# Performance work log

Hardware: AMD Instinct MI355X
Metric: run time of the kernel (lower is better)

Reference implementation:

```python
import jax, jax.numpy as jnp
import numpy as np
from jax import lax

B = 4096
IM = 64
HID = 256          # LSTM hidden
OBS_D = 400        # obs embedding dim
SAMP_D = 16        # sample embedding dim
ADDR_D = 16        # address embedding dim
IN_D = OBS_D + SAMP_D + ADDR_D  # 432 LSTM input dim


def setup_inputs() -> dict:
    key = jax.random.key(0)
    ks = jax.random.split(key, 32)
    n = jax.random.normal
    s = 0.05
    return {
        "obs": n(ks[0], (B, IM, IM), jnp.float32),
        "program_id": jax.random.randint(ks[1], (B,), 0, 3),
        "shape_id": jax.random.randint(ks[2], (B,), 0, 2),
        "shape_id_0": jax.random.randint(ks[3], (B,), 0, 2),
        "shape_id_1": jax.random.randint(ks[4], (B,), 0, 2),
        "eps_rp": n(ks[5], (B, 2), jnp.float32),
        "eps_rp0": n(ks[6], (B, 2), jnp.float32),
        "eps_rp1": n(ks[7], (B, 2), jnp.float32),
        # CNN obs embedder (stand-in for util.init_cnn(output_dim=16), flattening to 400)
        "conv1_w": n(ks[8], (32, 1, 3, 3)) * s,
        "conv1_b": n(ks[9], (32,)) * s,
        "conv2_w": n(ks[10], (16, 32, 3, 3)) * s,
        "conv2_b": n(ks[11], (16,)) * s,
        # raw_position_embedder: MLP 2 -> 100 -> 100 -> 16
        "mlp_w1": n(ks[12], (100, 2)) * s,
        "mlp_b1": n(ks[13], (100,)) * s,
        "mlp_w2": n(ks[14], (100, 100)) * s,
        "mlp_b2": n(ks[15], (100,)) * s,
        "mlp_w3": n(ks[16], (SAMP_D, 100)) * s,
        "mlp_b3": n(ks[17], (SAMP_D,)) * s,
        # LSTMCell params (PyTorch layout: [4H, in], gate order i,f,g,o)
        "W_ih": n(ks[18], (4 * HID, IN_D)) * s,
        "b_ih": n(ks[19], (4 * HID,)) * s,
        "W_hh": n(ks[20], (4 * HID, HID)) * s,
        "b_hh": n(ks[21], (4 * HID,)) * s,
        "addr_emb": n(ks[22], (7, ADDR_D)),
        "pid_emb": n(ks[23], (3, SAMP_D)),
        "sid_emb": n(ks[24], (2, SAMP_D)),
        "pid_ext_w": n(ks[25], (3, HID)) * s,
        "pid_ext_b": n(ks[26], (3,)) * s,
        "sid_ext_w": n(ks[27], (2, HID)) * s,
        "sid_ext_b": n(ks[28], (2,)) * s,
        "rp_ext_w": n(ks[29], (4, HID)) * s,
        "rp_ext_b": n(ks[30], (4,)) * s,
    }


def reference(obs, program_id, shape_id, shape_id_0, shape_id_1, eps_rp, eps_rp0, eps_rp1,
              conv1_w, conv1_b, conv2_w, conv2_b,
              mlp_w1, mlp_b1, mlp_w2, mlp_b2, mlp_w3, mlp_b3,
              W_ih, b_ih, W_hh, b_hh,
              addr_emb, pid_emb, sid_emb,
              pid_ext_w, pid_ext_b, sid_ext_w, sid_ext_b, rp_ext_w, rp_ext_b):
    b = obs.shape[0]
    # obs embedder: [B,1,64,64] -> conv s2 -> conv s2 -> avgpool 3x3 -> [B,16,5,5] -> [B,400]
    x = obs[:, None]
    x = jax.nn.relu(lax.conv_general_dilated(x, conv1_w, (2, 2), ((1, 1), (1, 1))) + conv1_b[None, :, None, None])
    x = jax.nn.relu(lax.conv_general_dilated(x, conv2_w, (2, 2), ((1, 1), (1, 1))) + conv2_b[None, :, None, None])
    x = lax.reduce_window(x, 0.0, lax.add, (1, 1, 3, 3), (1, 1, 3, 3), 'VALID') / 9.0
    obs_emb = x.reshape(b, OBS_D)

    def step(samp, aid, h, c):
        a = jnp.broadcast_to(addr_emb[aid], (b, ADDR_D))
        xin = jnp.concatenate([obs_emb, samp, a], axis=-1)
        g = xin @ W_ih.T + b_ih + h @ W_hh.T + b_hh
        i, f, gg, o = jnp.split(g, 4, axis=-1)
        c2 = jax.nn.sigmoid(f) * c + jax.nn.sigmoid(i) * jnp.tanh(gg)
        return jax.nn.sigmoid(o) * jnp.tanh(c2), c2

    zs = jnp.zeros((b, SAMP_D), obs.dtype)
    zh = jnp.zeros((b, HID), obs.dtype)
    h0, c0 = step(zs, 0, zh, zh)
    pid_logits = h0 @ pid_ext_w.T + pid_ext_b
    prev_pid = pid_emb[program_id]

    # branch 0 (program_id == 0): shape_id then raw_position
    h1, c1 = step(prev_pid, 1, h0, c0)
    sid_logits = h1 @ sid_ext_w.T + sid_ext_b
    h2, _ = step(sid_emb[shape_id], 4, h1, c1)
    rp = h2 @ rp_ext_w.T + rp_ext_b
    rp_b0 = rp[:, :2] + jnp.exp(rp[:, 2:]) * eps_rp

    # branch 1 (program_id != 0): shape_id_0, shape_id_1, raw_position_0, raw_position_1
    h1b, c1b = step(prev_pid, 2, h0, c0)
    sid0_logits = h1b @ sid_ext_w.T + sid_ext_b
    h2b, c2b = step(sid_emb[shape_id_0], 3, h1b, c1b)
    sid1_logits = h2b @ sid_ext_w.T + sid_ext_b
    h3b, c3b = step(sid_emb[shape_id_1], 5, h2b, c2b)
    rp0p = h3b @ rp_ext_w.T + rp_ext_b
    rp0 = rp0p[:, :2] + jnp.exp(rp0p[:, 2:]) * eps_rp0
    z = jnp.tanh(rp0 @ mlp_w1.T + mlp_b1)
    z = jnp.tanh(z @ mlp_w2.T + mlp_b2)
    rp0_emb = z @ mlp_w3.T + mlp_b3
    h4b, _ = step(rp0_emb, 6, h3b, c3b)
    rp1p = h4b @ rp_ext_w.T + rp_ext_b
    rp1 = rp1p[:, :2] + jnp.exp(rp1p[:, 2:]) * eps_rp1

    # [B, 3+2+2+2+2+2+2] = [B, 15]
    return jnp.concatenate([pid_logits, sid_logits, rp_b0, sid0_logits, sid1_logits, rp0, rp1], axis=-1)
```

## Files before the change

kernel.cpp:

```cpp
#include <hip/hip_runtime.h>
#include <hip/hip_bf16.h>
#include <math.h>

#define BATCH 4096
#define HID 256
#define OUT_W 15
#define AK 448

typedef unsigned short ushort_t;
typedef unsigned int uint_t;

using bf16x8 = __attribute__((ext_vector_type(8))) short;
using f32x4v = __attribute__((ext_vector_type(4))) float;
using f32x2 = __attribute__((ext_vector_type(2))) float;

__device__ __forceinline__ float sigf(float x) { return 1.0f / (1.0f + __expf(-x)); }
__device__ __forceinline__ float tanh_fast(float x) { return 1.0f - 2.0f / (__expf(2.0f * x) + 1.0f); }
__device__ __forceinline__ float bf2f(ushort_t u) { return __uint_as_float(((uint_t)u) << 16); }
__device__ __forceinline__ ushort_t f2bf(float x) {
    uint_t b = __float_as_uint(x);
    return (ushort_t)((b + 0x7fffu + ((b >> 16) & 1u)) >> 16);
}

__global__ __launch_bounds__(256) void prep_kernel(
// ... 108 lines not shown
    __shared__ __align__(16) float w1s[320];
    const int b = blockIdx.x, t = threadIdx.x;
    const float* og = obs + (size_t)b * 4096;

    const int w = t >> 6, L = t & 63, q = L >> 4, ln = L & 15;

    {
        uint_t* zE = (uint_t*)cE;
        uint_t* zO = (uint_t*)cO;
        for (int i = t; i < CE_RS / 2; i += 512) zE[i] = 0;
        for (int i = t; i < CO_RS / 2; i += 512) zO[i] = 0;
        if (t < 320) {
            int row = (t / 20) + 1, d = t % 20;
            zO[row * (CO_RS / 2) + d] = 0;
        }
    }
    if (t < 80) ((float4*)w1s)[t] = ((const float4*)w1pp)[t];
    if (t < 33) {
        int sw = (t >> 1) & 1;
        sm2[t * SM2S + sw * 4 + 3] = 0.f;
    }

    auto stage_obs = [&](int ph) {
        for (int i = t; i < 33 * 16; i += 512) {
            int row = i >> 4, c4 = i & 15;
            int sw = (row >> 1) & 1;
            int orow = 32 * ph - 1 + row;
            float4 v = float4{0.f, 0.f, 0.f, 0.f};
            if (orow >= 0) v = ((const float4*)(og + (size_t)orow * 64))[c4];
            *(float4*)&sm2[row * SM2S + ((1 + c4) ^ sw) * 4] = v;
        }
    };

    auto conv1_phase = [&](int ph) {
        const int r = t >> 5, g = (t >> 2) & 7, icq = t & 3;
        const int brow = ph ? r : (r + 1);
        float Pt[3][12];
        #pragma unroll
        for (int d = 0; d < 3; d++) {
            int row = 2 * r + d;
            int sw = (row >> 1) & 1;
            const float* base = &sm2[row * SM2S];
            #pragma unroll
            for (int j4 = 0; j4 < 3; j4++) {
                float4 v = *(const float4*)(base + ((2 * g + j4) ^ sw) * 4);
                Pt[d][j4 * 4 + 0] = v.x; Pt[d][j4 * 4 + 1] = v.y;
                Pt[d][j4 * 4 + 2] = v.z; Pt[d][j4 * 4 + 3] = v.w;
            }
        }
        const float* wpbase = &w1s[icq * 80];
        #pragma unroll
        for (int p = 0; p < 4; p++) {
            f32x2 pbc[9];
            #pragma unroll
            for (int d = 0; d < 3; d++)
                #pragma unroll
                for (int dx = 0; dx < 3; dx++) {
                    float v = Pt[d][2 * p + 3 + dx];
                    pbc[d * 3 + dx] = f32x2{v, v};
                }
            f32x2 sall[4];
            #pragma unroll
            for (int i = 0; i < 4; i++) {
                const float* wp = wpbase + i * 20;
                float4 wv0 = *(const float4*)(wp);
                float4 wv1 = *(const float4*)(wp + 4);
                float4 wv2 = *(const float4*)(wp + 8);
                float4 wv3 = *(const float4*)(wp + 12);
                float4 wv4 = *(const float4*)(wp + 16);
                f32x2 W2[10] = {f32x2{wv0.x, wv0.y}, f32x2{wv0.z, wv0.w},
                                f32x2{wv1.x, wv1.y}, f32x2{wv1.z, wv1.w},
                                f32x2{wv2.x, wv2.y}, f32x2{wv2.z, wv2.w},
                                f32x2{wv3.x, wv3.y}, f32x2{wv3.z, wv3.w},
                                f32x2{wv4.x, wv4.y}, f32x2{wv4.z, wv4.w}};
                f32x2 a2 = W2[9];
                #pragma unroll
                for (int k = 0; k < 9; k++)
                    a2 = __builtin_elementwise_fma(pbc[k], W2[k], a2);
                a2 = __builtin_elementwise_max(a2, f32x2{0.f, 0.f});
                sall[i] = a2;
            }
            uint_t d0, d1, d2, d3;
            asm("v_cvt_pk_bf16_f32 %0, %1, %2" : "=v"(d0) : "v"(sall[0].x), "v"(sall[1].x));
            asm("v_cvt_pk_bf16_f32 %0, %1, %2" : "=v"(d1) : "v"(sall[2].x), "v"(sall[3].x));
            asm("v_cvt_pk_bf16_f32 %0, %1, %2" : "=v"(d2) : "v"(sall[0].y), "v"(sall[1].y));
            asm("v_cvt_pk_bf16_f32 %0, %1, %2" : "=v"(d3) : "v"(sall[2].y), "v"(sall[3].y));
            int c = 4 * g + p;
            ushort_t* dst = (c & 1)
                ? &cO[brow * CO_RS + ((c + 1) >> 1) * 40 + icq * 8]
                : &cE[brow * CE_RS + (c >> 1) * 40 + icq * 8];
            *(uint4*)dst = uint4{d0, d1, d2, d3};
        }
    };

    auto conv2_phase = [&](int ph) {
        bf16x8 Bv[9];
        #pragma unroll
        for (int tap = 0; tap < 9; tap++)
            Bv[tap] = *reinterpret_cast<const bf16x8*>(&Btg[(tap * 16 + ln) * 32 + q * 8]);
        const int y = 8 * ph + w;
        f32x4v C = {0.f, 0.f, 0.f, 0.f};
        #pragma unroll
        for (int dy = 0; dy < 3; dy++) {
            int br = 2 * y + dy;
            if (br >= 17) br -= 17;
            bf16x8 a0 = *reinterpret_cast<const bf16x8*>(&cO[br * CO_RS + ln * 40 + q * 8]);
            bf16x8 a1 = *reinterpret_cast<const bf16x8*>(&cE[br * CE_RS + ln * 40 + q * 8]);
            bf16x8 a2 = *reinterpret_cast<const bf16x8*>(&cO[br * CO_RS + (ln + 1) * 40 + q * 8]);
            C = __builtin_amdgcn_mfma_f32_16x16x32_bf16(a0, Bv[dy * 3 + 0], C, 0, 0, 0);
            C = __builtin_amdgcn_mfma_f32_16x16x32_bf16(a1, Bv[dy * 3 + 1], C, 0, 0, 0);
            C = __builtin_amdgcn_mfma_f32_16x16x32_bf16(a2, Bv[dy * 3 + 2], C, 0, 0, 0);
        }
        float bb2 = b2[ln];
        float4 o;
        o.x = fmaxf(C[0] + bb2, 0.f);
        o.y = fmaxf(C[1] + bb2, 0.f);
        o.z = fmaxf(C[2] + bb2, 0.f);
        o.w = fmaxf(C[3] + bb2, 0.f);
        *(float4*)&c2s[ln * C2S_CS + y * C2S_RS + q * 4] = o;
    };

    stage_obs(0);
    __syncthreads();
    conv1_phase(0);
    __syncthreads();
    stage_obs(1);
    conv2_phase(0);
    __syncthreads();
    conv1_phase(1);
    __syncthreads();
    conv2_phase(1);
    __syncthreads();

    ushort_t* ew = (ushort_t*)w1s;
    if (t < 400) {
        int c = t / 25, rem = t % 25, py = rem / 5, px = rem % 5;
        float s = 0.f;
        #pragma unroll
        for (int dy = 0; dy < 3; dy++)
            #pragma unroll
            for (int dx = 0; dx < 3; dx++)
                s += c2s[c * C2S_CS + (3 * py + dy) * C2S_RS + 3 * px + dx];
        ew[t] = f2bf(s * (1.f / 9.f));
    } else if (t < AK) {
        ew[t] = 0;
    }
    __syncthreads();
    if (t < 56)
        ((uint4*)(obs_emb_b + (size_t)b * AK))[t] = ((const uint4*)ew)[t];
}

__global__ __launch_bounds__(256) void obs_gemm(
    const ushort_t* __restrict__ Ab, const ushort_t* __restrict__ Wob,
    ushort_t* __restrict__ outp, const float* __restrict__ bias0,
    float* __restrict__ c0_out, ushort_t* __restrict__ hb0_out)
{
    __shared__ __align__(16) ushort_t As[64 * 72];
    __shared__ __align__(16) ushort_t ob[64 * 132];
    const int t = threadIdx.x;
    const int bm = blockIdx.x & 63, bu = blockIdx.x >> 6;
    const int b0 = bm * 64, U0 = bu * 32;
    const int w = t >> 6, L = t & 63, q = L >> 4, ln = L & 15;
    const int m0 = w * 16;

    f32x4v acc[8];
    #pragma unroll
    for (int i = 0; i < 8; i++) acc[i] = f32x4v{0.f, 0.f, 0.f, 0.f};

    for (int kc = 0; kc < 7; kc++) {
        #pragma unroll
        for (int ii = 0; ii < 2; ii++) {
            int i = t + ii * 256;
            int row = i >> 3, c8 = i & 7;
            *(uint4*)&As[row * 72 + c8 * 8] =
                *(const uint4*)&Ab[(size_t)(b0 + row) * AK + kc * 64 + c8 * 8];
        }
        __syncthreads();
        bf16x8 a[2];
        #pragma unroll
        for (int ks = 0; ks < 2; ks++)
            a[ks] = *reinterpret_cast<const bf16x8*>(&As[(m0 + ln) * 72 + ks * 32 + q * 8]);
        #pragma unroll
        for (int ct = 0; ct < 8; ct++) {
            int col = (ct >> 1) * 256 + U0 + (ct & 1) * 16 + ln;
            const ushort_t* wr = Wob + (size_t)col * AK + kc * 64 + q * 8;
            bf16x8 bv0 = *reinterpret_cast<const bf16x8*>(wr);
            bf16x8 bv1 = *reinterpret_cast<const bf16x8*>(wr + 32);
            acc[ct] = __builtin_amdgcn_mfma_f32_16x16x32_bf16(a[0], bv0, acc[ct], 0, 0, 0);
            acc[ct] = __builtin_amdgcn_mfma_f32_16x16x32_bf16(a[1], bv1, acc[ct], 0, 0, 0);
        }
        __syncthreads();
    }

    #pragma unroll
    for (int h = 0; h < 2; h++) {
        const int u = U0 + h * 16 + ln;
        float bg[4];
        #pragma unroll
        for (int g = 0; g < 4; g++) bg[g] = bias0[g * 256 + u];
        #pragma unroll
        for (int j = 0; j < 4; j++) {
            int row = b0 + m0 + q * 4 + j;
            float pre[4];
            #pragma unroll
            for (int g = 0; g < 4; g++) pre[g] = acc[g * 2 + h][j] + bg[g];
            float c2 = sigf(pre[0]) * tanh_fast(pre[2]);
            float hv = sigf(pre[3]) * tanh_fast(c2);
            c0_out[(size_t)row * 256 + u] = c2;
            hb0_out[(size_t)row * 256 + u] = f2bf(hv);
        }
    }

    #pragma unroll
    for (int ct = 0; ct < 8; ct++)
        #pragma unroll
        for (int j = 0; j < 4; j++)
            ob[(m0 + q * 4 + j) * 132 + ct * 16 + ln] = f2bf(acc[ct][j]);
    __syncthreads();
    #pragma unroll
    for (int p2 = 0; p2 < 4; p2++) {
        int idx = t + p2 * 256;
        int row = idx >> 4, c8 = idx & 15;
        int cl = c8 * 8;
        int gcol = (cl >> 5) * 256 + U0 + ((cl >> 4) & 1) * 16 + (cl & 15);
        uint4 v = *(const uint4*)&ob[row * 132 + cl];
        *(uint4*)&outp[(size_t)(b0 + row) * 1024 + gcol] = v;
    }
}

template <int SAMP, int HEAD_N, int DUAL>
__global__ __launch_bounds__(512, 4) void lstm_mfma(
    const ushort_t* __restrict__ hb_in, const float* __restrict__ c_in,
    ushort_t* __restrict__ hb_out, float* __restrict__ c_out,
    const ushort_t* __restrict__ obs_part, const float* __restrict__ bias_s,
    const float* __restrict__ samp_rows, const int* __restrict__ samp_idx,
    const float* __restrict__ rp0_emb, const float* __restrict__ WsampT,
    const ushort_t* __restrict__ Wb,
    const float* __restrict__ head_w, const float* __restrict__ head_b,
    float* __restrict__ out, int out_off,
    const ushort_t* __restrict__ hb_in2, const float* __restrict__ c_in2,
    ushort_t* __restrict__ hb_out2, float* __restrict__ c_out2,
    const float* __restrict__ bias_s2, const int* __restrict__ samp_idx2,
    const float* __restrict__ head_w2, int out_off2)
{
    constexpr int PS_B = 64 * 132 * 2;
    constexpr int CS_B = 64 * 36 * 4;
    constexpr int EX_B = (SAMP == 2) ? (16 * 132 * 4 + 64 * 20 * 4)
                                     : (3 * 256 * 4 + 64 * 8 * 3 * 4);
    __shared__ __align__(16) char smem[PS_B + CS_B + EX_B];
    ushort_t* ps = (ushort_t*)smem;
    float* cs = (float*)(smem + PS_B);
    float* hws = (float*)(smem + PS_B + CS_B);
    float* red = (float*)(smem + PS_B + CS_B + 3 * 256 * 4);
    float* wsmp = (float*)(smem + PS_B + CS_B);
    float* re = (float*)(smem + PS_B + CS_B + 16 * 132 * 4);

    const int t = threadIdx.x;
    const int half  = DUAL ? (int)(blockIdx.x >> 9) : 0;
    const int inner = DUAL ? (int)(blockIdx.x & 511) : (int)blockIdx.x;
    const int bm = inner & 63, bu = inner >> 6;
    const int b0 = bm * 64;

    const ushort_t* hbi = (DUAL && half) ? hb_in2 : hb_in;
    const float* cip    = (DUAL && half) ? c_in2 : c_in;
    ushort_t* hbo       = (DUAL && half) ? hb_out2 : hb_out;
    float* cop          = (DUAL && half) ? c_out2 : c_out;
    const float* biasp  = (DUAL && half) ? bias_s2 : bias_s;
    const int* sidx     = (DUAL && half) ? samp_idx2 : samp_idx;
    const float* hwp    = (DUAL && half) ? head_w2 : head_w;
    const int ooff      = (DUAL && half) ? out_off2 : out_off;
    const bool do_head  = (HEAD_N > 0) && (bu == 0) && (hwp != nullptr);

    const int w = t >> 6, L = t & 63, q = L >> 4, ln = L & 15;
    const int m0 = (w & 3) * 16, wg = w >> 2;
    const int U0 = bu * 32;
    const int unit = U0 + wg * 16 + ln;

    bf16x8 a[8];
    {
        const ushort_t* arow = hbi + (size_t)(b0 + m0 + ln) * 256 + q * 8;
        #pragma unroll
        for (int kk = 0; kk < 8; kk++)
            a[kk] = *reinterpret_cast<const bf16x8*>(arow + kk * 32);
    }

    #pragma unroll
    for (int p = 0; p < 2; p++) {
        int idx = t + p * 512;
        int row = idx >> 4, c8 = idx & 15;
        int g = c8 >> 2, cc = (c8 & 3) * 8;
        uint4 v = *(const uint4*)&obs_part[(size_t)(b0 + row) * 1024 + g * 256 + U0 + cc];
        *(uint4*)&ps[row * 132 + c8 * 8] = v;
    }
    {
        int row = t >> 3, c4 = t & 7;
        float4 v = *(const float4*)&cip[(size_t)(b0 + row) * 256 + U0 + c4 * 4];
        *(float4*)&cs[row * 36 + c4 * 4] = v;
    }
    if (SAMP == 2) {
        int k = t >> 5, c4 = t & 31;
        float4 v = *(const float4*)&WsampT[(size_t)k * 1024 + ((c4 * 4) >> 5) * 256 + U0 + ((c4 * 4) & 31)];
        *(float4*)&wsmp[k * 132 + c4 * 4] = v;
        if (t < 256) {
            int row = t >> 2, d4 = t & 3;
            float4 e = *(const float4*)&rp0_emb[(size_t)(b0 + row) * 16 + d4 * 4];
            *(float4*)&re[row * 20 + d4 * 4] = e;
        }
    }
    if (do_head)
        for (int i = t; i < HEAD_N * 256; i += 512) hws[i] = hwp[i];

    f32x4v acc[4];
    #pragma unroll
    for (int g = 0; g < 4; g++) {
        f32x4v z = {0.f, 0.f, 0.f, 0.f};
        const ushort_t* wrow = Wb + (size_t)(g * 256 + unit) * 256 + q * 8;
        #pragma unroll
        for (int kk = 0; kk < 8; kk++) {
            bf16x8 bv = *reinterpret_cast<const bf16x8*>(wrow + kk * 32);
            z = __builtin_amdgcn_mfma_f32_16x16x32_bf16(a[kk], bv, z, 0, 0, 0);
        }
        acc[g] = z;
    }
    __syncthreads();

    float bsv[4];
    #pragma unroll
    for (int g = 0; g < 4; g++) bsv[g] = biasp[g * 256 + unit];

    const int cc = wg * 16 + ln;
    #pragma unroll
    for (int r = 0; r < 4; r++) {
        const int row = m0 + q * 4 + r;
        const int R = b0 + row;
        float pre[4];
        #pragma unroll
        for (int g = 0; g < 4; g++)
            pre[g] = acc[g][r] + bf2f(ps[row * 132 + g * 32 + cc]) + bsv[g];
        if (SAMP == 1) {
            int si = sidx[R];
            #pragma unroll
            for (int g = 0; g < 4; g++) pre[g] += samp_rows[si * 1024 + g * 256 + unit];
        }
        if (SAMP == 2) {
            #pragma unroll
            for (int k = 0; k < 16; k++) {
                float e = re[row * 20 + k];
                #pragma unroll
                for (int g = 0; g < 4; g++) pre[g] += e * wsmp[k * 132 + g * 32 + cc];
            }
        }
        float ci = cs[row * 36 + cc];
        float c2 = sigf(pre[1]) * ci + sigf(pre[0]) * tanh_fast(pre[2]);
        float hv = sigf(pre[3]) * tanh_fast(c2);
        cs[row * 36 + cc] = c2;
        ps[row * 132 + cc] = f2bf(hv);
    }
    __syncthreads();

    {
        int row = t >> 3, c4 = t & 7;
        float4 v = *(const float4*)&cs[row * 36 + c4 * 4];
        *(float4*)&cop[(size_t)(b0 + row) * 256 + U0 + c4 * 4] = v;
    }
    if (t < 256) {
        int row = t >> 2, c8 = t & 3;
        uint4 v = *(const uint4*)&ps[row * 132 + c8 * 8];
        *(uint4*)&hbo[(size_t)(b0 + row) * 256 + U0 + c8 * 8] = v;
    }

    if (do_head) {
        const int row = t >> 3, seg = t & 7;
        const ushort_t* hrow = hbi + (size_t)(b0 + row) * 256 + seg * 32;
        float part[3] = {0.f, 0.f, 0.f};
        #pragma unroll
        for (int j = 0; j < 4; j++) {
            uint4 v = *(const uint4*)(hrow + j * 8);
            uint_t dw[4] = {v.x, v.y, v.z, v.w};
            #pragma unroll
            for (int d = 0; d < 4; d++) {
                float f0 = __uint_as_float(dw[d] << 16);
                float f1 = __uint_as_float(dw[d] & 0xffff0000u);
                int k = seg * 32 + j * 8 + d * 2;
                #pragma unroll
                for (int n = 0; n < HEAD_N; n++)
                    part[n] += f0 * hws[n * 256 + k] + f1 * hws[n * 256 + k + 1];
            }
        }
        #pragma unroll
        for (int n = 0; n < HEAD_N; n++) red[(row * 8 + seg) * 3 + n] = part[n];
        __syncthreads();
        if (t < 64) {
            #pragma unroll
            for (int n = 0; n < HEAD_N; n++) {
                float s = head_b[n];
                #pragma unroll
                for (int p = 0; p < 8; p++) s += red[(t * 8 + p) * 3 + n];
                out[(size_t)(b0 + t) * OUT_W + ooff + n] = s;
            }
        }
    }
}

__global__ __launch_bounds__(256) void rp_head(
    const ushort_t* __restrict__ hb, const float* __restrict__ head_w,
    const float* __restrict__ head_b, const float* __restrict__ eps,
    float* __restrict__ out, int out_off, float* __restrict__ rp_store)
{
    __shared__ float hw[1024];
    __shared__ float red[16 * 16 * 4];
    __shared__ float sred[16 * 4];
    const int t = threadIdx.x;
    const int b0 = blockIdx.x * 16;
    for (int i = t; i < 1024; i += 256) hw[i] = head_w[i];
    __syncthreads();
    const int r = t >> 4, p = t & 15;
    {
        const int R = b0 + r;
        float part[4] = {0.f, 0.f, 0.f, 0.f};
        const ushort_t* hr = hb + (size_t)R * 256 + p * 16;
        #pragma unroll
        for (int j = 0; j < 2; j++) {
            uint4 v = *reinterpret_cast<const uint4*>(hr + j * 8);
            uint_t dw[4] = {v.x, v.y, v.z, v.w};
            #pragma unroll
            for (int d = 0; d < 4; d++) {
                float f0 = __uint_as_float(dw[d] << 16);
                float f1 = __uint_as_float(dw[d] & 0xffff0000u);
                int k = p * 16 + j * 8 + d * 2;
                #pragma unroll
                for (int n = 0; n < 4; n++)
                    part[n] += f0 * hw[n * 256 + k] + f1 * hw[n * 256 + k + 1];
            }
        }
        #pragma unroll
        for (int n = 0; n < 4; n++) red[(r * 16 + p) * 4 + n] = part[n];
    }
    __syncthreads();
    if (t < 64) {
        int row = t >> 2, n = t & 3;
        float s = head_b[n];
        #pragma unroll
        for (int p2 = 0; p2 < 16; p2++) s += red[(row * 16 + p2) * 4 + n];
        sred[row * 4 + n] = s;
    }
    __syncthreads();
    if (t < 16) {
        const int R = b0 + t;
        float s0 = sred[t * 4 + 0], s1 = sred[t * 4 + 1];
        float s2 = sred[t * 4 + 2], s3 = sred[t * 4 + 3];
        float v0 = s0 + __expf(s2) * eps[(size_t)R * 2 + 0];
        float v1 = s1 + __expf(s3) * eps[(size_t)R * 2 + 1];
        out[(size_t)R * OUT_W + out_off + 0] = v0;
        out[(size_t)R * OUT_W + out_off + 1] = v1;
        if (rp_store) {
            rp_store[(size_t)R * 2 + 0] = v0;
            rp_store[(size_t)R * 2 + 1] = v1;
        }
    }
}

__global__ __launch_bounds__(128) void mlp_kernel(
    const float* __restrict__ rp0, const float* __restrict__ w1,
    const float* __restrict__ b1, const float* __restrict__ w2t,
    const float* __restrict__ b2, const float* __restrict__ w3t,
    const float* __restrict__ b3, float* __restrict__ emb)
{
    __shared__ float z1[100], z2[100];
    int row = blockIdx.x, t = threadIdx.x;
    float r0 = rp0[(size_t)row * 2], r1 = rp0[(size_t)row * 2 + 1];
    if (t < 100) z1[t] = tanh_fast(b1[t] + w1[t * 2] * r0 + w1[t * 2 + 1] * r1);
    __syncthreads();
    if (t < 100) {
        float s = b2[t];
        for (int k = 0; k < 100; k++) s += w2t[k * 100 + t] * z1[k];
        z2[t] = tanh_fast(s);
    }
    __syncthreads();
    if (t < 16) {
        float s = b3[t];
        for (int k = 0; k < 100; k++) s += w3t[k * 16 + t] * z2[k];
        emb[(size_t)row * 16 + t] = s;
    }
}

extern "C" void kernel_launch(void* const* d_in, const int* in_sizes, int n_in,
                              void* d_out, int out_size, void* d_ws, size_t ws_size,
                              hipStream_t stream)
{
    const float* obs        = (const float*)d_in[0];
    const int*   program_id = (const int*)d_in[1];
    const int*   shape_id   = (const int*)d_in[2];
    const int*   shape_id_0 = (const int*)d_in[3];
    const int*   shape_id_1 = (const int*)d_in[4];
    const float* eps_rp     = (const float*)d_in[5];
    const float* eps_rp0    = (const float*)d_in[6];
    const float* eps_rp1    = (const float*)d_in[7];
    const float* conv1_w    = (const float*)d_in[8];
    const float* conv1_b    = (const float*)d_in[9];
    const float* conv2_w    = (const float*)d_in[10];
    const float* conv2_b    = (const float*)d_in[11];
    const float* mlp_w1     = (const float*)d_in[12];
    const float* mlp_b1     = (const float*)d_in[13];
    const float* mlp_w2     = (const float*)d_in[14];
    const float* mlp_b2     = (const float*)d_in[15];
    const float* mlp_w3     = (const float*)d_in[16];
    const float* mlp_b3     = (const float*)d_in[17];
    const float* W_ih       = (const float*)d_in[18];
    const float* b_ih       = (const float*)d_in[19];
    const float* W_hh       = (const float*)d_in[20];
    const float* b_hh       = (const float*)d_in[21];
    const float* addr_emb   = (const float*)d_in[22];
    const float* pid_emb    = (const float*)d_in[23];
    const float* sid_emb    = (const float*)d_in[24];
    const float* pid_ext_w  = (const float*)d_in[25];
    const float* pid_ext_b  = (const float*)d_in[26];
    const float* sid_ext_w  = (const float*)d_in[27];
    const float* sid_ext_b  = (const float*)d_in[28];
    const float* rp_ext_w   = (const float*)d_in[29];
    const float* rp_ext_b   = (const float*)d_in[30];
    float* out = (float*)d_out;

    float* ws = (float*)d_ws;
    size_t off = 0;
    float* W_ih_T   = ws + off; off += 432 * 1024;
    ushort_t* Wb    = (ushort_t*)(ws + off); off += 131072;
    float* bias_all = ws + off; off += 7 * 1024;
    float* pid_rows = ws + off; off += 3 * 1024;
    float* sid_rows = ws + off; off += 2 * 1024;
    ushort_t* obs_emb_b = (ushort_t*)(ws + off); off += (size_t)BATCH * AK / 2;
    ushort_t* Wobs_b    = (ushort_t*)(ws + off); off += (size_t)1024 * AK / 2;
    ushort_t* obs_part = (ushort_t*)(ws + off); off += (size_t)BATCH * 512;
    ushort_t* hb0 = (ushort_t*)(ws + off); off += (size_t)BATCH * 128;
    ushort_t* hbA = (ushort_t*)(ws + off); off += (size_t)BATCH * 128;
    ushort_t* hbB = (ushort_t*)(ws + off); off += (size_t)BATCH * 128;
    ushort_t* hbC = (ushort_t*)(ws + off); off += (size_t)BATCH * 128;
    ushort_t* hbA2 = (ushort_t*)(ws + off); off += (size_t)BATCH * 128;
    ushort_t* hbB2 = (ushort_t*)(ws + off); off += (size_t)BATCH * 128;
    float* c0 = ws + off; off += (size_t)BATCH * 256;
    float* cA = ws + off; off += (size_t)BATCH * 256;
    float* cB = ws + off; off += (size_t)BATCH * 256;
    float* cC = ws + off; off += (size_t)BATCH * 256;
    float* cD = ws + off; off += (size_t)BATCH * 256;
    float* cA2 = ws + off; off += (size_t)BATCH * 256;
    float* rp0      = ws + off; off += (size_t)BATCH * 2;
    float* rp0_emb  = ws + off; off += (size_t)BATCH * 16;
    float* w2t = ws + off; off += 10000;
    float* w3t = ws + off; off += 1600;
    float* w1pp = ws + off; off += 384;
    ushort_t* Btg = (ushort_t*)(ws + off); off += 2304;
    float* WsampT = W_ih_T + (size_t)400 * 1024;

    prep_kernel<<<68, 256, 0, stream>>>(W_ih, W_hh, b_ih, b_hh, addr_emb,
                                        pid_emb, sid_emb, mlp_w2, mlp_w3,
                                        conv1_w, conv1_b, conv2_w,
                                        W_ih_T, Wb, bias_all, pid_rows,
                                        sid_rows, w2t, w3t, w1pp, Btg, Wobs_b);
    conv_kernel<<<BATCH, 512, 0, stream>>>(obs, w1pp, Btg, conv2_b, obs_emb_b);
    obs_gemm<<<512, 256, 0, stream>>>(obs_emb_b, Wobs_b, obs_part,
                                      bias_all + 0 * 1024, c0, hb0);

    lstm_mfma<1, 3, 1><<<1024, 512, 0, stream>>>(
        hb0, c0, hbA, cA, obs_part, bias_all + 1 * 1024,
        pid_rows, program_id, nullptr, nullptr, Wb,
        pid_ext_w, pid_ext_b, out, 0,
        hb0, c0, hbA2, cA2, bias_all + 3 * 1024, program_id, nullptr, 0);
    lstm_mfma<1, 2, 1><<<1024, 512, 0, stream>>>(
        hbA, cA, hbB, cD, obs_part, bias_all + 2 * 1024,
        sid_rows, shape_id, nullptr, nullptr, Wb,
        sid_ext_w, sid_ext_b, out, 3,
        hbA2, cA2, hbB2, cB, bias_all + 4 * 1024, shape_id_0, sid_ext_w, 7);
    rp_head<<<256, 256, 0, stream>>>(hbB, rp_ext_w, rp_ext_b, eps_rp, out, 5, nullptr);
    lstm_mfma<1, 2, 0><<<512, 512, 0, stream>>>(
        hbB2, cB, hbC, cC, obs_part, bias_all + 5 * 1024,
        sid_rows, shape_id_1, nullptr, nullptr, Wb,
        sid_ext_w, sid_ext_b, out, 9,
        nullptr, nullptr, nullptr, nullptr, nullptr, nullptr, nullptr, 0);
    rp_head<<<256, 256, 0, stream>>>(hbC, rp_ext_w, rp_ext_b, eps_rp0, out, 11, rp0);
    mlp_kernel<<<BATCH, 128, 0, stream>>>(rp0, mlp_w1, mlp_b1, w2t, mlp_b2,
                                          w3t, mlp_b3, rp0_emb);
    lstm_mfma<2, 0, 0><<<512, 512, 0, stream>>>(
        hbC, cC, hbB, cD, obs_part, bias_all + 6 * 1024,
        nullptr, nullptr, rp0_emb, WsampT, Wb,
        nullptr, nullptr, out, 0,
        nullptr, nullptr, nullptr, nullptr, nullptr, nullptr, nullptr, 0);
    rp_head<<<256, 256, 0, stream>>>(hbB, rp_ext_w, rp_ext_b, eps_rp1, out, 13, nullptr);
}
```

Before: 424.8 us.

## Fuse the whole LSTM step chain, heads and MLP into one persistent kernel

```diff
diff --git a/kernel.cpp b/kernel.cpp
--- a/kernel.cpp
+++ b/kernel.cpp
@@ -284,14 +284,13 @@
 
 __global__ __launch_bounds__(256) void obs_gemm(
     const ushort_t* __restrict__ Ab, const ushort_t* __restrict__ Wob,
-    ushort_t* __restrict__ outp, const float* __restrict__ bias0,
-    float* __restrict__ c0_out, ushort_t* __restrict__ hb0_out)
+    ushort_t* __restrict__ outp)
 {
     __shared__ __align__(16) ushort_t As[64 * 72];
     __shared__ __align__(16) ushort_t ob[64 * 132];
     const int t = threadIdx.x;
     const int bm = blockIdx.x & 63, bu = blockIdx.x >> 6;
-    const int b0 = bm * 64, U0 = bu * 32;
+    const int b0 = bm * 64, n0 = bu * 128;
     const int w = t >> 6, L = t & 63, q = L >> 4, ln = L & 15;
     const int m0 = w * 16;
 
@@ -314,8 +313,7 @@
             a[ks] = *reinterpret_cast<const bf16x8*>(&As[(m0 + ln) * 72 + ks * 32 + q * 8]);
         #pragma unroll
         for (int ct = 0; ct < 8; ct++) {
-            int col = (ct >> 1) * 256 + U0 + (ct & 1) * 16 + ln;
-            const ushort_t* wr = Wob + (size_t)col * AK + kc * 64 + q * 8;
+            const ushort_t* wr = Wob + (size_t)(n0 + ct * 16 + ln) * AK + kc * 64 + q * 8;
             bf16x8 bv0 = *reinterpret_cast<const bf16x8*>(wr);
             bf16x8 bv1 = *reinterpret_cast<const bf16x8*>(wr + 32);
             acc[ct] = __builtin_amdgcn_mfma_f32_16x16x32_bf16(a[0], bv0, acc[ct], 0, 0, 0);
@@ -323,26 +321,6 @@
         }
         __syncthreads();
     }
-
-    #pragma unroll
-    for (int h = 0; h < 2; h++) {
-        const int u = U0 + h * 16 + ln;
-        float bg[4];
-        #pragma unroll
-        for (int g = 0; g < 4; g++) bg[g] = bias0[g * 256 + u];
-        #pragma unroll
-        for (int j = 0; j < 4; j++) {
-            int row = b0 + m0 + q * 4 + j;
-            float pre[4];
-            #pragma unroll
-            for (int g = 0; g < 4; g++) pre[g] = acc[g * 2 + h][j] + bg[g];
-            float c2 = sigf(pre[0]) * tanh_fast(pre[2]);
-            float hv = sigf(pre[3]) * tanh_fast(c2);
-            c0_out[(size_t)row * 256 + u] = c2;
-            hb0_out[(size_t)row * 256 + u] = f2bf(hv);
-        }
-    }
-
     #pragma unroll
     for (int ct = 0; ct < 8; ct++)
         #pragma unroll
@@ -353,267 +331,283 @@
     for (int p2 = 0; p2 < 4; p2++) {
         int idx = t + p2 * 256;
         int row = idx >> 4, c8 = idx & 15;
-        int cl = c8 * 8;
-        int gcol = (cl >> 5) * 256 + U0 + ((cl >> 4) & 1) * 16 + (cl & 15);
-        uint4 v = *(const uint4*)&ob[row * 132 + cl];
-        *(uint4*)&outp[(size_t)(b0 + row) * 1024 + gcol] = v;
-    }
-}
-
-template <int SAMP, int HEAD_N, int DUAL>
-__global__ __launch_bounds__(512, 4) void lstm_mfma(
-    const ushort_t* __restrict__ hb_in, const float* __restrict__ c_in,
-    ushort_t* __restrict__ hb_out, float* __restrict__ c_out,
-    const ushort_t* __restrict__ obs_part, const float* __restrict__ bias_s,
-    const float* __restrict__ samp_rows, const int* __restrict__ samp_idx,
-    const float* __restrict__ rp0_emb, const float* __restrict__ WsampT,
-    const ushort_t* __restrict__ Wb,
-    const float* __restrict__ head_w, const float* __restrict__ head_b,
-    float* __restrict__ out, int out_off,
-    const ushort_t* __restrict__ hb_in2, const float* __restrict__ c_in2,
-    ushort_t* __restrict__ hb_out2, float* __restrict__ c_out2,
-    const float* __restrict__ bias_s2, const int* __restrict__ samp_idx2,
-    const float* __restrict__ head_w2, int out_off2)
+        uint4 v = *(const uint4*)&ob[row * 132 + c8 * 8];
+        *(uint4*)&outp[(size_t)(b0 + row) * 1024 + n0 + c8 * 8] = v;
+    }
+}
+
+template <int N>
+__device__ __forceinline__ void head_logits_f(
+    const ushort_t* hsrc, const float* __restrict__ hw, const float* __restrict__ hb,
+    int off, float* red, float* __restrict__ out, int b0, int t)
 {
-    constexpr int PS_B = 64 * 132 * 2;
-    constexpr int CS_B = 64 * 36 * 4;
-    constexpr int EX_B = (SAMP == 2) ? (16 * 132 * 4 + 64 * 20 * 4)
-                                     : (3 * 256 * 4 + 64 * 8 * 3 * 4);
-    __shared__ __align__(16) char smem[PS_B + CS_B + EX_B];
-    ushort_t* ps = (ushort_t*)smem;
-    float* cs = (float*)(smem + PS_B);
-    float* hws = (float*)(smem + PS_B + CS_B);
-    float* red = (float*)(smem + PS_B + CS_B + 3 * 256 * 4);
-    float* wsmp = (float*)(smem + PS_B + CS_B);
-    float* re = (float*)(smem + PS_B + CS_B + 16 * 132 * 4);
-
-    const int t = threadIdx.x;
-    const int half  = DUAL ? (int)(blockIdx.x >> 9) : 0;
-    const int inner = DUAL ? (int)(blockIdx.x & 511) : (int)blockIdx.x;
-    const int bm = inner & 63, bu = inner >> 6;
-    const int b0 = bm * 64;
-
-    const ushort_t* hbi = (DUAL && half) ? hb_in2 : hb_in;
-    const float* cip    = (DUAL && half) ? c_in2 : c_in;
-    ushort_t* hbo       = (DUAL && half) ? hb_out2 : hb_out;
-    float* cop          = (DUAL && half) ? c_out2 : c_out;
-    const float* biasp  = (DUAL && half) ? bias_s2 : bias_s;
-    const int* sidx     = (DUAL && half) ? samp_idx2 : samp_idx;
-    const float* hwp    = (DUAL && half) ? head_w2 : head_w;
-    const int ooff      = (DUAL && half) ? out_off2 : out_off;
-    const bool do_head  = (HEAD_N > 0) && (bu == 0) && (hwp != nullptr);
-
-    const int w = t >> 6, L = t & 63, q = L >> 4, ln = L & 15;
-    const int m0 = (w & 3) * 16, wg = w >> 2;
-    const int U0 = bu * 32;
-    const int unit = U0 + wg * 16 + ln;
-
-    bf16x8 a[8];
-    {
-        const ushort_t* arow = hbi + (size_t)(b0 + m0 + ln) * 256 + q * 8;
-        #pragma unroll
-        for (int kk = 0; kk < 8; kk++)
-            a[kk] = *reinterpret_cast<const bf16x8*>(arow + kk * 32);
-    }
-
-    #pragma unroll
-    for (int p = 0; p < 2; p++) {
-        int idx = t + p * 512;
-        int row = idx >> 4, c8 = idx & 15;
-        int g = c8 >> 2, cc = (c8 & 3) * 8;
-        uint4 v = *(const uint4*)&obs_part[(size_t)(b0 + row) * 1024 + g * 256 + U0 + cc];
-        *(uint4*)&ps[row * 132 + c8 * 8] = v;
-    }
-    {
-        int row = t >> 3, c4 = t & 7;
-        float4 v = *(const float4*)&cip[(size_t)(b0 + row) * 256 + U0 + c4 * 4];
-        *(float4*)&cs[row * 36 + c4 * 4] = v;
-    }
-    if (SAMP == 2) {
-        int k = t >> 5, c4 = t & 31;
-        float4 v = *(const float4*)&WsampT[(size_t)k * 1024 + ((c4 * 4) >> 5) * 256 + U0 + ((c4 * 4) & 31)];
-        *(float4*)&wsmp[k * 132 + c4 * 4] = v;
-        if (t < 256) {
-            int row = t >> 2, d4 = t & 3;
-            float4 e = *(const float4*)&rp0_emb[(size_t)(b0 + row) * 16 + d4 * 4];
-            *(float4*)&re[row * 20 + d4 * 4] = e;
-        }
-    }
-    if (do_head)
-        for (int i = t; i < HEAD_N * 256; i += 512) hws[i] = hwp[i];
-
-    f32x4v acc[4];
-    #pragma unroll
-    for (int g = 0; g < 4; g++) {
-        f32x4v z = {0.f, 0.f, 0.f, 0.f};
-        const ushort_t* wrow = Wb + (size_t)(g * 256 + unit) * 256 + q * 8;
-        #pragma unroll
-        for (int kk = 0; kk < 8; kk++) {
-            bf16x8 bv = *reinterpret_cast<const bf16x8*>(wrow + kk * 32);
-            z = __builtin_amdgcn_mfma_f32_16x16x32_bf16(a[kk], bv, z, 0, 0, 0);
-        }
-        acc[g] = z;
-    }
-    __syncthreads();
-
-    float bsv[4];
-    #pragma unroll
-    for (int g = 0; g < 4; g++) bsv[g] = biasp[g * 256 + unit];
-
-    const int cc = wg * 16 + ln;
-    #pragma unroll
-    for (int r = 0; r < 4; r++) {
-        const int row = m0 + q * 4 + r;
-        const int R = b0 + row;
-        float pre[4];
-        #pragma unroll
-        for (int g = 0; g < 4; g++)
-            pre[g] = acc[g][r] + bf2f(ps[row * 132 + g * 32 + cc]) + bsv[g];
-        if (SAMP == 1) {
-            int si = sidx[R];
-            #pragma unroll
-            for (int g = 0; g < 4; g++) pre[g] += samp_rows[si * 1024 + g * 256 + unit];
-        }
-        if (SAMP == 2) {
-            #pragma unroll
-            for (int k = 0; k < 16; k++) {
-                float e = re[row * 20 + k];
-                #pragma unroll
-                for (int g = 0; g < 4; g++) pre[g] += e * wsmp[k * 132 + g * 32 + cc];
-            }
-        }
-        float ci = cs[row * 36 + cc];
-        float c2 = sigf(pre[1]) * ci + sigf(pre[0]) * tanh_fast(pre[2]);
-        float hv = sigf(pre[3]) * tanh_fast(c2);
-        cs[row * 36 + cc] = c2;
-        ps[row * 132 + cc] = f2bf(hv);
-    }
-    __syncthreads();
-
-    {
-        int row = t >> 3, c4 = t & 7;
-        float4 v = *(const float4*)&cs[row * 36 + c4 * 4];
-        *(float4*)&cop[(size_t)(b0 + row) * 256 + U0 + c4 * 4] = v;
-    }
-    if (t < 256) {
-        int row = t >> 2, c8 = t & 3;
-        uint4 v = *(const uint4*)&ps[row * 132 + c8 * 8];
-        *(uint4*)&hbo[(size_t)(b0 + row) * 256 + U0 + c8 * 8] = v;
-    }
-
-    if (do_head) {
-        const int row = t >> 3, seg = t & 7;
-        const ushort_t* hrow = hbi + (size_t)(b0 + row) * 256 + seg * 32;
-        float part[3] = {0.f, 0.f, 0.f};
-        #pragma unroll
-        for (int j = 0; j < 4; j++) {
-            uint4 v = *(const uint4*)(hrow + j * 8);
-            uint_t dw[4] = {v.x, v.y, v.z, v.w};
-            #pragma unroll
-            for (int d = 0; d < 4; d++) {
-                float f0 = __uint_as_float(dw[d] << 16);
-                float f1 = __uint_as_float(dw[d] & 0xffff0000u);
-                int k = seg * 32 + j * 8 + d * 2;
-                #pragma unroll
-                for (int n = 0; n < HEAD_N; n++)
-                    part[n] += f0 * hws[n * 256 + k] + f1 * hws[n * 256 + k + 1];
-            }
-        }
-        #pragma unroll
-        for (int n = 0; n < HEAD_N; n++) red[(row * 8 + seg) * 3 + n] = part[n];
-        __syncthreads();
-        if (t < 64) {
-            #pragma unroll
-            for (int n = 0; n < HEAD_N; n++) {
-                float s = head_b[n];
-                #pragma unroll
-                for (int p = 0; p < 8; p++) s += red[(t * 8 + p) * 3 + n];
-                out[(size_t)(b0 + t) * OUT_W + ooff + n] = s;
-            }
-        }
-    }
-}
-
-__global__ __launch_bounds__(256) void rp_head(
-    const ushort_t* __restrict__ hb, const float* __restrict__ head_w,
-    const float* __restrict__ head_b, const float* __restrict__ eps,
-    float* __restrict__ out, int out_off, float* __restrict__ rp_store)
+    const int row = t >> 5, seg = t & 31;
+    float part[N] = {};
+    const ushort_t* hr = hsrc + row * 272 + seg * 8;
+    #pragma unroll
+    for (int e = 0; e < 8; e++) {
+        float hv = bf2f(hr[e]);
+        #pragma unroll
+        for (int m = 0; m < N; m++) part[m] += hv * hw[m * 256 + seg * 8 + e];
+    }
+    #pragma unroll
+    for (int m = 0; m < N; m++) red[(row * 32 + seg) * 4 + m] = part[m];
+    __syncthreads();
+    if (t < 16 * N) {
+        int r2 = t / N, m = t % N;
+        float s = hb[m];
+        for (int p = 0; p < 32; p++) s += red[(r2 * 32 + p) * 4 + m];
+        out[(size_t)(b0 + r2) * OUT_W + off + m] = s;
+    }
+    __syncthreads();
+}
+
+__device__ __forceinline__ void head_rp_f(
+    const ushort_t* hsrc, const float* __restrict__ hw, const float* __restrict__ hb,
+    const float* __restrict__ eps, int off, float* red, float* hdr,
+    float* __restrict__ out, float* rp0s, int b0, int t)
 {
-    __shared__ float hw[1024];
-    __shared__ float red[16 * 16 * 4];
-    __shared__ float sred[16 * 4];
+    const int row = t >> 5, seg = t & 31;
+    float part[4] = {0.f, 0.f, 0.f, 0.f};
+    const ushort_t* hr = hsrc + row * 272 + seg * 8;
+    #pragma unroll
+    for (int e = 0; e < 8; e++) {
+        float hv = bf2f(hr[e]);
+        #pragma unroll
+        for (int m = 0; m < 4; m++) part[m] += hv * hw[m * 256 + seg * 8 + e];
+    }
+    #pragma unroll
+    for (int m = 0; m < 4; m++) red[(row * 32 + seg) * 4 + m] = part[m];
+    __syncthreads();
+    if (t < 64) {
+        int r2 = t >> 2, m = t & 3;
+        float s = hb[m];
+        for (int p = 0; p < 32; p++) s += red[(r2 * 32 + p) * 4 + m];
+        hdr[t] = s;
+    }
+    __syncthreads();
+    if (t < 16) {
+        int R = b0 + t;
+        float v0 = hdr[t * 4 + 0] + __expf(hdr[t * 4 + 2]) * eps[(size_t)R * 2 + 0];
+        float v1 = hdr[t * 4 + 1] + __expf(hdr[t * 4 + 3]) * eps[(size_t)R * 2 + 1];
+        out[(size_t)R * OUT_W + off + 0] = v0;
+        out[(size_t)R * OUT_W + off + 1] = v1;
+        if (rp0s) { rp0s[t * 2 + 0] = v0; rp0s[t * 2 + 1] = v1; }
+    }
+    __syncthreads();
+}
+
+__global__ __launch_bounds__(512, 2) void lstm_chain(
+    const ushort_t* __restrict__ obs_part, const float* __restrict__ bias_all,
+    const float* __restrict__ pid_rows, const float* __restrict__ sid_rows,
+    const int* __restrict__ program_id, const int* __restrict__ shape_id,
+    const int* __restrict__ shape_id_0, const int* __restrict__ shape_id_1,
+    const ushort_t* __restrict__ Wb, const float* __restrict__ WsampT,
+    const float* __restrict__ pid_ext_w, const float* __restrict__ pid_ext_b,
+    const float* __restrict__ sid_ext_w, const float* __restrict__ sid_ext_b,
+    const float* __restrict__ rp_ext_w, const float* __restrict__ rp_ext_b,
+    const float* __restrict__ eps_rp, const float* __restrict__ eps_rp0,
+    const float* __restrict__ eps_rp1,
+    const float* __restrict__ mlp_w1, const float* __restrict__ mlp_b1,
+    const float* __restrict__ w2t, const float* __restrict__ mlp_b2,
+    const float* __restrict__ w3t, const float* __restrict__ mlp_b3,
+    float* __restrict__ out)
+{
+    __shared__ __align__(16) ushort_t ps_t[1024 * 20];
+    __shared__ __align__(16) ushort_t hbuf[3][16 * 272];
+    __shared__ float red[16 * 32 * 4];
+    __shared__ float hdr[64];
+    __shared__ float z1s[16][104], z2s[16][104];
+    __shared__ float emb_s[16][20];
+    __shared__ float rp0s[16][2];
+    __shared__ int sidx_s[4][16];
+
     const int t = threadIdx.x;
     const int b0 = blockIdx.x * 16;
-    for (int i = t; i < 1024; i += 256) hw[i] = head_w[i];
-    __syncthreads();
-    const int r = t >> 4, p = t & 15;
-    {
-        const int R = b0 + r;
-        float part[4] = {0.f, 0.f, 0.f, 0.f};
-        const ushort_t* hr = hb + (size_t)R * 256 + p * 16;
-        #pragma unroll
-        for (int j = 0; j < 2; j++) {
-            uint4 v = *reinterpret_cast<const uint4*>(hr + j * 8);
-            uint_t dw[4] = {v.x, v.y, v.z, v.w};
-            #pragma unroll
-            for (int d = 0; d < 4; d++) {
-                float f0 = __uint_as_float(dw[d] << 16);
-                float f1 = __uint_as_float(dw[d] & 0xffff0000u);
-                int k = p * 16 + j * 8 + d * 2;
-                #pragma unroll
-                for (int n = 0; n < 4; n++)
-                    part[n] += f0 * hw[n * 256 + k] + f1 * hw[n * 256 + k + 1];
-            }
-        }
-        #pragma unroll
-        for (int n = 0; n < 4; n++) red[(r * 16 + p) * 4 + n] = part[n];
-    }
-    __syncthreads();
+    const int w = t >> 6, L = t & 63, q = L >> 4, ln = L & 15;
+    const int U = w * 32;
+
     if (t < 64) {
-        int row = t >> 2, n = t & 3;
-        float s = head_b[n];
-        #pragma unroll
-        for (int p2 = 0; p2 < 16; p2++) s += red[(row * 16 + p2) * 4 + n];
-        sred[row * 4 + n] = s;
-    }
-    __syncthreads();
-    if (t < 16) {
-        const int R = b0 + t;
-        float s0 = sred[t * 4 + 0], s1 = sred[t * 4 + 1];
-        float s2 = sred[t * 4 + 2], s3 = sred[t * 4 + 3];
-        float v0 = s0 + __expf(s2) * eps[(size_t)R * 2 + 0];
-        float v1 = s1 + __expf(s3) * eps[(size_t)R * 2 + 1];
-        out[(size_t)R * OUT_W + out_off + 0] = v0;
-        out[(size_t)R * OUT_W + out_off + 1] = v1;
-        if (rp_store) {
-            rp_store[(size_t)R * 2 + 0] = v0;
-            rp_store[(size_t)R * 2 + 1] = v1;
-        }
-    }
-}
-
-__global__ __launch_bounds__(128) void mlp_kernel(
-    const float* __restrict__ rp0, const float* __restrict__ w1,
-    const float* __restrict__ b1, const float* __restrict__ w2t,
-    const float* __restrict__ b2, const float* __restrict__ w3t,
-    const float* __restrict__ b3, float* __restrict__ emb)
-{
-    __shared__ float z1[100], z2[100];
-    int row = blockIdx.x, t = threadIdx.x;
-    float r0 = rp0[(size_t)row * 2], r1 = rp0[(size_t)row * 2 + 1];
-    if (t < 100) z1[t] = tanh_fast(b1[t] + w1[t * 2] * r0 + w1[t * 2 + 1] * r1);
-    __syncthreads();
-    if (t < 100) {
-        float s = b2[t];
-        for (int k = 0; k < 100; k++) s += w2t[k * 100 + t] * z1[k];
-        z2[t] = tanh_fast(s);
-    }
-    __syncthreads();
-    if (t < 16) {
-        float s = b3[t];
-        for (int k = 0; k < 100; k++) s += w3t[k * 16 + t] * z2[k];
-        emb[(size_t)row * 16 + t] = s;
-    }
+        int tbl = t >> 4, r = t & 15;
+        const int* src = (tbl == 0) ? program_id : (tbl == 1) ? shape_id
+                       : (tbl == 2) ? shape_id_0 : shape_id_1;
+        sidx_s[tbl][r] = src[b0 + r];
+    }
+    for (int i = t; i < 2048; i += 512) {
+        int row = i >> 7, c8 = (i & 127) * 8;
+        uint4 v = *(const uint4*)&obs_part[(size_t)(b0 + row) * 1024 + c8];
+        uint_t dw[4] = {v.x, v.y, v.z, v.w};
+        #pragma unroll
+        for (int k = 0; k < 4; k++) {
+            ps_t[(c8 + 2 * k) * 20 + row] = (ushort_t)(dw[k] & 0xffffu);
+            ps_t[(c8 + 2 * k + 1) * 20 + row] = (ushort_t)(dw[k] >> 16);
+        }
+    }
+    __syncthreads();
+
+    float cA[8], cB[8];
+    f32x4v acc[4][2];
+
+    #pragma unroll
+    for (int h = 0; h < 2; h++) {
+        const int unit = U + h * 16 + ln;
+        float pre[4][4];
+        #pragma unroll
+        for (int g = 0; g < 4; g++) {
+            uint2 pv = *(const uint2*)&ps_t[(g * 256 + unit) * 20 + q * 4];
+            float bg = bias_all[g * 256 + unit];
+            pre[g][0] = bf2f((ushort_t)(pv.x & 0xffffu)) + bg;
+            pre[g][1] = bf2f((ushort_t)(pv.x >> 16)) + bg;
+            pre[g][2] = bf2f((ushort_t)(pv.y & 0xffffu)) + bg;
+            pre[g][3] = bf2f((ushort_t)(pv.y >> 16)) + bg;
+        }
+        #pragma unroll
+        for (int j = 0; j < 4; j++) {
+            float c2 = sigf(pre[0][j]) * tanh_fast(pre[2][j]);
+            float hv = sigf(pre[3][j]) * tanh_fast(c2);
+            cA[j * 2 + h] = c2; cB[j * 2 + h] = c2;
+            hbuf[0][(q * 4 + j) * 272 + unit] = f2bf(hv);
+        }
+    }
+    __syncthreads();
+
+    auto gemm = [&](int src) {
+        bf16x8 a[8];
+        #pragma unroll
+        for (int kk = 0; kk < 8; kk++)
+            a[kk] = *reinterpret_cast<const bf16x8*>(&hbuf[src][ln * 272 + kk * 32 + q * 8]);
+        #pragma unroll
+        for (int g = 0; g < 4; g++)
+            #pragma unroll
+            for (int h = 0; h < 2; h++) {
+                f32x4v z = {0.f, 0.f, 0.f, 0.f};
+                const ushort_t* wr = Wb + (size_t)(g * 256 + U + h * 16 + ln) * 256 + q * 8;
+                #pragma unroll
+                for (int kk = 0; kk < 8; kk++)
+                    z = __builtin_amdgcn_mfma_f32_16x16x32_bf16(a[kk],
+                        *reinterpret_cast<const bf16x8*>(wr + kk * 32), z, 0, 0, 0);
+                acc[g][h] = z;
+            }
+    };
+
+    auto epi = [&](int bi, const float* samp, int tbl, int dst, float* cr) {
+        #pragma unroll
+        for (int h = 0; h < 2; h++) {
+            const int unit = U + h * 16 + ln;
+            float pre[4][4];
+            #pragma unroll
+            for (int g = 0; g < 4; g++) {
+                uint2 pv = *(const uint2*)&ps_t[(g * 256 + unit) * 20 + q * 4];
+                float bg = bias_all[bi * 1024 + g * 256 + unit];
+                pre[g][0] = acc[g][h][0] + bf2f((ushort_t)(pv.x & 0xffffu)) + bg;
+                pre[g][1] = acc[g][h][1] + bf2f((ushort_t)(pv.x >> 16)) + bg;
+                pre[g][2] = acc[g][h][2] + bf2f((ushort_t)(pv.y & 0xffffu)) + bg;
+                pre[g][3] = acc[g][h][3] + bf2f((ushort_t)(pv.y >> 16)) + bg;
+            }
+            #pragma unroll
+            for (int j = 0; j < 4; j++) {
+                int si = sidx_s[tbl][q * 4 + j];
+                #pragma unroll
+                for (int g = 0; g < 4; g++)
+                    pre[g][j] += samp[(size_t)si * 1024 + g * 256 + unit];
+            }
+            #pragma unroll
+            for (int j = 0; j < 4; j++) {
+                float ci = cr[j * 2 + h];
+                float c2 = sigf(pre[1][j]) * ci + sigf(pre[0][j]) * tanh_fast(pre[2][j]);
+                float hv = sigf(pre[3][j]) * tanh_fast(c2);
+                cr[j * 2 + h] = c2;
+                hbuf[dst][(q * 4 + j) * 272 + unit] = f2bf(hv);
+            }
+        }
+    };
+
+    head_logits_f<3>(hbuf[0], pid_ext_w, pid_ext_b, 0, red, out, b0, t);
+
+    gemm(0);
+    epi(1, pid_rows, 0, 1, cA);
+    epi(3, pid_rows, 0, 2, cB);
+    __syncthreads();
+
+    head_logits_f<2>(hbuf[1], sid_ext_w, sid_ext_b, 3, red, out, b0, t);
+
+    gemm(1);
+    epi(2, sid_rows, 1, 0, cA);
+    __syncthreads();
+
+    head_rp_f(hbuf[0], rp_ext_w, rp_ext_b, eps_rp, 5, red, hdr, out, nullptr, b0, t);
+
+    gemm(2);
+    epi(4, sid_rows, 2, 1, cB);
+    __syncthreads();
+
+    head_logits_f<2>(hbuf[2], sid_ext_w, sid_ext_b, 7, red, out, b0, t);
+    head_logits_f<2>(hbuf[1], sid_ext_w, sid_ext_b, 9, red, out, b0, t);
+
+    gemm(1);
+    epi(5, sid_rows, 3, 2, cB);
+    __syncthreads();
+
+    head_rp_f(hbuf[2], rp_ext_w, rp_ext_b, eps_rp0, 11, red, hdr, out, &rp0s[0][0], b0, t);
+
+    for (int i = t; i < 1600; i += 512) {
+        int row = i / 100, j = i % 100;
+        z1s[row][j] = tanh_fast(mlp_b1[j] + mlp_w1[j * 2] * rp0s[row][0]
+                                          + mlp_w1[j * 2 + 1] * rp0s[row][1]);
+    }
+    __syncthreads();
+    for (int i = t; i < 1600; i += 512) {
+        int row = i / 100, j = i % 100;
+        float s = mlp_b2[j];
+        for (int k = 0; k < 100; k++) s += w2t[k * 100 + j] * z1s[row][k];
+        z2s[row][j] = tanh_fast(s);
+    }
+    __syncthreads();
+    if (t < 256) {
+        int row = t >> 4, o = t & 15;
+        float s = mlp_b3[o];
+        for (int k = 0; k < 100; k++) s += w3t[k * 16 + o] * z2s[row][k];
+        emb_s[row][o] = s;
+    }
+    __syncthreads();
+
+    gemm(2);
+    #pragma unroll
+    for (int h = 0; h < 2; h++) {
+        const int unit = U + h * 16 + ln;
+        float pre[4][4];
+        #pragma unroll
+        for (int g = 0; g < 4; g++) {
+            uint2 pv = *(const uint2*)&ps_t[(g * 256 + unit) * 20 + q * 4];
+            float bg = bias_all[6 * 1024 + g * 256 + unit];
+            pre[g][0] = acc[g][h][0] + bf2f((ushort_t)(pv.x & 0xffffu)) + bg;
+            pre[g][1] = acc[g][h][1] + bf2f((ushort_t)(pv.x >> 16)) + bg;
+            pre[g][2] = acc[g][h][2] + bf2f((ushort_t)(pv.y & 0xffffu)) + bg;
+            pre[g][3] = acc[g][h][3] + bf2f((ushort_t)(pv.y >> 16)) + bg;
+        }
+        #pragma unroll
+        for (int k = 0; k < 16; k++) {
+            float wv[4];
+            #pragma unroll
+            for (int g = 0; g < 4; g++) wv[g] = WsampT[(size_t)k * 1024 + g * 256 + unit];
+            #pragma unroll
+            for (int j = 0; j < 4; j++) {
+                float e = emb_s[q * 4 + j][k];
+                #pragma unroll
+                for (int g = 0; g < 4; g++) pre[g][j] += e * wv[g];
+            }
+        }
+        #pragma unroll
+        for (int j = 0; j < 4; j++) {
+            float ci = cB[j * 2 + h];
+            float c2 = sigf(pre[1][j]) * ci + sigf(pre[0][j]) * tanh_fast(pre[2][j]);
+            float hv = sigf(pre[3][j]) * tanh_fast(c2);
+            hbuf[0][(q * 4 + j) * 272 + unit] = f2bf(hv);
+        }
+    }
+    __syncthreads();
+
+    head_rp_f(hbuf[0], rp_ext_w, rp_ext_b, eps_rp1, 13, red, hdr, out, nullptr, b0, t);
 }
 
 extern "C" void kernel_launch(void* const* d_in, const int* in_sizes, int n_in,
@@ -663,20 +657,6 @@
     ushort_t* obs_emb_b = (ushort_t*)(ws + off); off += (size_t)BATCH * AK / 2;
     ushort_t* Wobs_b    = (ushort_t*)(ws + off); off += (size_t)1024 * AK / 2;
     ushort_t* obs_part = (ushort_t*)(ws + off); off += (size_t)BATCH * 512;
-    ushort_t* hb0 = (ushort_t*)(ws + off); off += (size_t)BATCH * 128;
-    ushort_t* hbA = (ushort_t*)(ws + off); off += (size_t)BATCH * 128;
-    ushort_t* hbB = (ushort_t*)(ws + off); off += (size_t)BATCH * 128;
-    ushort_t* hbC = (ushort_t*)(ws + off); off += (size_t)BATCH * 128;
-    ushort_t* hbA2 = (ushort_t*)(ws + off); off += (size_t)BATCH * 128;
-    ushort_t* hbB2 = (ushort_t*)(ws + off); off += (size_t)BATCH * 128;
-    float* c0 = ws + off; off += (size_t)BATCH * 256;
-    float* cA = ws + off; off += (size_t)BATCH * 256;
-    float* cB = ws + off; off += (size_t)BATCH * 256;
-    float* cC = ws + off; off += (size_t)BATCH * 256;
-    float* cD = ws + off; off += (size_t)BATCH * 256;
-    float* cA2 = ws + off; off += (size_t)BATCH * 256;
-    float* rp0      = ws + off; off += (size_t)BATCH * 2;
-    float* rp0_emb  = ws + off; off += (size_t)BATCH * 16;
     float* w2t = ws + off; off += 10000;
     float* w3t = ws + off; off += 1600;
     float* w1pp = ws + off; off += 384;
@@ -689,32 +669,11 @@
                                         W_ih_T, Wb, bias_all, pid_rows,
                                         sid_rows, w2t, w3t, w1pp, Btg, Wobs_b);
     conv_kernel<<<BATCH, 512, 0, stream>>>(obs, w1pp, Btg, conv2_b, obs_emb_b);
-    obs_gemm<<<512, 256, 0, stream>>>(obs_emb_b, Wobs_b, obs_part,
-                                      bias_all + 0 * 1024, c0, hb0);
-
-    lstm_mfma<1, 3, 1><<<1024, 512, 0, stream>>>(
-        hb0, c0, hbA, cA, obs_part, bias_all + 1 * 1024,
-        pid_rows, program_id, nullptr, nullptr, Wb,
-        pid_ext_w, pid_ext_b, out, 0,
-        hb0, c0, hbA2, cA2, bias_all + 3 * 1024, program_id, nullptr, 0);
-    lstm_mfma<1, 2, 1><<<1024, 512, 0, stream>>>(
-        hbA, cA, hbB, cD, obs_part, bias_all + 2 * 1024,
-        sid_rows, shape_id, nullptr, nullptr, Wb,
-        sid_ext_w, sid_ext_b, out, 3,
-        hbA2, cA2, hbB2, cB, bias_all + 4 * 1024, shape_id_0, sid_ext_w, 7);
-    rp_head<<<256, 256, 0, stream>>>(hbB, rp_ext_w, rp_ext_b, eps_rp, out, 5, nullptr);
-    lstm_mfma<1, 2, 0><<<512, 512, 0, stream>>>(
-        hbB2, cB, hbC, cC, obs_part, bias_all + 5 * 1024,
-        sid_rows, shape_id_1, nullptr, nullptr, Wb,
-        sid_ext_w, sid_ext_b, out, 9,
-        nullptr, nullptr, nullptr, nullptr, nullptr, nullptr, nullptr, 0);
-    rp_head<<<256, 256, 0, stream>>>(hbC, rp_ext_w, rp_ext_b, eps_rp0, out, 11, rp0);
-    mlp_kernel<<<BATCH, 128, 0, stream>>>(rp0, mlp_w1, mlp_b1, w2t, mlp_b2,
-                                          w3t, mlp_b3, rp0_emb);
-    lstm_mfma<2, 0, 0><<<512, 512, 0, stream>>>(
-        hbC, cC, hbB, cD, obs_part, bias_all + 6 * 1024,
-        nullptr, nullptr, rp0_emb, WsampT, Wb,
-        nullptr, nullptr, out, 0,
-        nullptr, nullptr, nullptr, nullptr, nullptr, nullptr, nullptr, 0);
-    rp_head<<<256, 256, 0, stream>>>(hbB, rp_ext_w, rp_ext_b, eps_rp1, out, 13, nullptr);
-}
+    obs_gemm<<<512, 256, 0, stream>>>(obs_emb_b, Wobs_b, obs_part);
+    lstm_chain<<<256, 512, 0, stream>>>(
+        obs_part, bias_all, pid_rows, sid_rows,
+        program_id, shape_id, shape_id_0, shape_id_1, Wb, WsampT,
+        pid_ext_w, pid_ext_b, sid_ext_w, sid_ext_b, rp_ext_w, rp_ext_b,
+        eps_rp, eps_rp0, eps_rp1,
+        mlp_w1, mlp_b1, w2t, mlp_b2, w3t, mlp_b3, out);
+}
```

After: 382.3 us. 10.0% less time.
